# Kernel optimization log

Measured on AMD Instinct MI355X. Metric: run time of the kernel, lower is better.

Reference implementation:

```python
import jax, jax.numpy as jnp
import numpy as np

R = 100        # voxel grid resolution per axis
N = 200000     # number of active (non-empty) voxels
K = 3          # kernel size
CIN = 64
COUT = 64
NOFF = K ** 3 - 1  # 26 non-center offsets


def _build_maps():
    # Mirrors mapping_cuda: per kernel offset, find (input_row, output_row) pairs
    # such that coords[input] == coords[output] + offset (submanifold conv,
    # output coords == input coords).
    rng = np.random.default_rng(0)
    lin = rng.choice(R ** 3, size=N, replace=False)
    coords = np.stack(np.unravel_index(lin, (R, R, R)), axis=1)  # [N,3]
    lut = np.full(R ** 3, -1, dtype=np.int64)
    lut[lin] = np.arange(N)
    offs = [(dx, dy, dz) for dx in (-1, 0, 1) for dy in (-1, 0, 1)
            for dz in (-1, 0, 1) if (dx, dy, dz) != (0, 0, 0)]
    ins, outs = [], []
    for d in offs:
        tgt = coords - np.asarray(d)              # output coord receiving input i
        valid = np.all((tgt >= 0) & (tgt < R), axis=1)
        idx_i = np.nonzero(valid)[0]
        tlin = np.ravel_multi_index(tgt[valid].T, (R, R, R))
        j = lut[tlin]
        hit = j >= 0
        ins.append(idx_i[hit].astype(np.int32))
        outs.append(j[hit].astype(np.int32))
    P = max(len(a) for a in ins)
    imap = np.full((NOFF, P), -1, dtype=np.int32)
    omap = np.full((NOFF, P), -1, dtype=np.int32)
    for k, (a, b) in enumerate(zip(ins, outs)):
        imap[k, :len(a)] = a
        omap[k, :len(b)] = b
    return jnp.asarray(imap), jnp.asarray(omap)


def setup_inputs() -> dict:
    key = jax.random.key(0)
    kf, kw = jax.random.split(key)
    feats = jax.random.normal(kf, (N, CIN), dtype=jnp.float32)
    # reset_parameters: uniform(-stdv, stdv), stdv = 1/sqrt(out_channels * K^3)
    stdv = 1.0 / float(np.sqrt(COUT * K ** 3))
    kernel = jax.random.uniform(kw, (K ** 3, CIN, COUT), dtype=jnp.float32,
                                minval=-stdv, maxval=stdv)
    imap, omap = _build_maps()
    return {"feats": feats, "kernel": kernel, "imap": imap, "omap": omap}


def reference(feats, kernel, imap, omap):
    # Submanifold sparse 3D conv: gather -> per-offset GEMM -> scatter-add.
    K3 = kernel.shape[0]
    c = K3 // 2  # center offset: identity neighbor map
    w_nc = jnp.concatenate([kernel[:c], kernel[c + 1:]], axis=0)  # [26,Cin,Cout]
    mask = imap >= 0                                   # [26,P]
    gath = feats[jnp.where(mask, imap, 0)] * mask[..., None]   # [26,P,Cin]
    y = jnp.einsum('kpc,kco->kpo', gath, w_nc)         # [26,P,Cout]
    out = feats @ kernel[c]                            # center contribution [N,Cout]
    oi = jnp.where(mask, omap, 0).reshape(-1)          # masked rows add zeros at row 0
    out = out.at[oi].add(y.reshape(-1, y.shape[-1]))
    return out
```

## Files before the change

### kernel.cpp

```cpp
#include <hip/hip_runtime.h>


#define CIN 64
#define COUT 64
#define TR 32
#define NOFF 26

typedef short bf16x8 __attribute__((ext_vector_type(8)));
typedef unsigned short ushort8 __attribute__((ext_vector_type(8)));
typedef float f32x4 __attribute__((ext_vector_type(4)));

__device__ inline unsigned short bfbits(float f) {
    unsigned u = __builtin_bit_cast(unsigned, f);
    u += 0x7fffu + ((u >> 16) & 1u);
    return (unsigned short)(u >> 16);
}

__device__ inline int kk_of_item(int i) {
    return (i >= 26) ? 13 : 26 - (i < 13 ? i : i + 1);
}

__global__ __launch_bounds__(256) void prep_feats(const float* __restrict__ f,
                                                  unsigned short* __restrict__ fb,
                                                  int n) {
    const int i8 = (blockIdx.x * 256 + threadIdx.x) * 8;
    if (i8 >= n) return;
    const float4 v0 = *(const float4*)(f + i8);
    const float4 v1 = *(const float4*)(f + i8 + 4);
    union { unsigned short u[8]; bf16x8 v; } r;
    r.u[0] = bfbits(v0.x); r.u[1] = bfbits(v0.y);
    r.u[2] = bfbits(v0.z); r.u[3] = bfbits(v0.w);
    r.u[4] = bfbits(v1.x); r.u[5] = bfbits(v1.y);
    r.u[6] = bfbits(v1.z); r.u[7] = bfbits(v1.w);
    *(bf16x8*)(fb + i8) = r.v;
}

__global__ __launch_bounds__(256) void prep_wt(const float* __restrict__ W,
                                               unsigned short* __restrict__ Wt) {
    const int k = blockIdx.x;
    for (int idx = threadIdx.x; idx < CIN * COUT; idx += 256) {
        const int c = idx >> 6, o = idx & 63;
        const int q = c >> 3, e = c & 7;
        Wt[((k * 64 + o) * 64) + (((q ^ (o & 7)) << 3) + e)] =
            bfbits(W[(k * 64 + c) * 64 + o]);
    }
}

__global__ __launch_bounds__(256) void prep_tab_init(int* __restrict__ tab,
                                                     int nt, int N) {
    const size_t i4 = ((size_t)blockIdx.x * 256 + threadIdx.x) * 4;
    const size_t total = (size_t)27 * nt * TR;
    if (i4 >= total) return;
    const size_t mstep = (size_t)nt * TR;
    int4 v;
    int* vp = (int*)&v;
#pragma unroll
    for (int e = 0; e < 4; ++e) {
        const size_t l = i4 + e;
        const int m = (int)(l / mstep);
        const int r = (int)(l - (size_t)m * mstep);
        vp[e] = (m == 26 && r < N) ? r : N;
    }
    *(int4*)(tab + i4) = v;
}

__global__ __launch_bounds__(256) void prep_tab(const int* __restrict__ imap,
                                                const int* __restrict__ omap,
                                                int P, int nt,
                                                int* __restrict__ tab) {
    const int p = blockIdx.x * 256 + threadIdx.x;
    const int m = blockIdx.y;
    if (p >= P) return;
    const int iv = imap[(size_t)m * P + p];
    if (iv < 0) return;
    tab[((size_t)m * nt + (iv >> 5)) * TR + (iv & 31)] = omap[(size_t)m * P + p];
}

__global__ __launch_bounds__(256, 4) void spconv_v7(
    const unsigned short* __restrict__ fb,
    const unsigned short* __restrict__ wt,
    const int* __restrict__ tab,
    float* __restrict__ out, int N, int nt, int nwg)
{
    __shared__ unsigned short wbuf[2][4096];

    const int tid = threadIdx.x, w = tid >> 6, lane = tid & 63;
    const int col = lane & 15, grp = lane >> 4;

    const int orig = blockIdx.x;
    const int q = nwg >> 3, r8 = nwg & 7;
    const int xcd = orig & 7, k = orig >> 3;
    const int sb = (xcd < r8 ? xcd * (q + 1) : r8 * (q + 1) + (xcd - r8) * q) + k;

    const int t = sb * 4 + w;
    const int tt = (t < nt) ? t : (nt - 1);
    const int r0 = t * TR;
    const size_t tstep = (size_t)nt * TR;
    const int* tb = tab + (size_t)tt * TR + col;

#define TAB(j, s) tb[(size_t)((j) < 27 ? (j) : 26) * tstep + (s) * 16]

    int sv1[2], sv2[2], tvA[2], tvB[2];
    bf16x8 a0[2][2], a1[2][2], a2[2][2];
#pragma unroll
    for (int s = 0; s < 2; ++s) {
        const int sv0 = TAB(0, s);
        sv1[s] = TAB(1, s);
        sv2[s] = TAB(2, s);
        tvA[s] = TAB(3, s);
        tvB[s] = TAB(4, s);
        const bf16x8* fp = (const bf16x8*)(fb + (size_t)sv0 * 64 + grp * 8);
        a0[s][0] = fp[0];
        a0[s][1] = fp[4];
        const bf16x8* fq = (const bf16x8*)(fb + (size_t)sv1[s] * 64 + grp * 8);
        a1[s][0] = fq[0];
        a1[s][1] = fq[4];
    }

    {
        const unsigned short* wk = wt + kk_of_item(0) * 4096;
        const ushort8 wl0 = *(const ushort8*)(wk + tid * 8);
        const ushort8 wl1 = *(const ushort8*)(wk + 2048 + tid * 8);
        *(ushort8*)(&wbuf[0][tid * 8]) = wl0;
        *(ushort8*)(&wbuf[0][2048 + tid * 8]) = wl1;
    }
    asm volatile("s_waitcnt lgkmcnt(0)" ::: "memory");
    __builtin_amdgcn_s_barrier();

    f32x4 acc[2][4];
#pragma unroll
    for (int s = 0; s < 2; ++s)
#pragma unroll
        for (int ot = 0; ot < 4; ++ot) acc[s][ot] = {0.f, 0.f, 0.f, 0.f};

    for (int it = 0; it < 27; ++it) {
        const unsigned short* wkn = wt + kk_of_item(it + 1) * 4096;
        const ushort8 wl0 = *(const ushort8*)(wkn + tid * 8);
        const ushort8 wl1 = *(const ushort8*)(wkn + 2048 + tid * 8);

#pragma unroll
        for (int s = 0; s < 2; ++s) {
            const bf16x8* fp = (const bf16x8*)(fb + (size_t)sv2[s] * 64 + grp * 8);
            a2[s][0] = fp[0];
            a2[s][1] = fp[4];
        }

        int svn[2];
#pragma unroll
        for (int s = 0; s < 2; ++s) {
            svn[s] = tvA[s];
            tvA[s] = tvB[s];
            tvB[s] = TAB(it + 5, s);
        }

        const unsigned short* cb = wbuf[it & 1];
        __builtin_amdgcn_s_setprio(1);
#pragma unroll
        for (int ot = 0; ot < 4; ++ot) {
            const int o = ot * 16 + col;
            const bf16x8 b0 = *(const bf16x8*)(cb + o * 64 + ((grp ^ (col & 7)) << 3));
            const bf16x8 b1 = *(const bf16x8*)(cb + o * 64 + (((4 + grp) ^ (col & 7)) << 3));
#pragma unroll
            for (int s = 0; s < 2; ++s) {
                acc[s][ot] = __builtin_amdgcn_mfma_f32_16x16x32_bf16(a0[s][0], b0, acc[s][ot], 0, 0, 0);
                acc[s][ot] = __builtin_amdgcn_mfma_f32_16x16x32_bf16(a0[s][1], b1, acc[s][ot], 0, 0, 0);
            }
        }
        __builtin_amdgcn_s_setprio(0);

        unsigned short* nb = wbuf[(it + 1) & 1];
        *(ushort8*)(&nb[tid * 8]) = wl0;
        *(ushort8*)(&nb[2048 + tid * 8]) = wl1;

        asm volatile("s_waitcnt lgkmcnt(0)" ::: "memory");
        __builtin_amdgcn_s_barrier();

#pragma unroll
        for (int s = 0; s < 2; ++s) {
            a0[s][0] = a1[s][0]; a0[s][1] = a1[s][1];
            a1[s][0] = a2[s][0]; a1[s][1] = a2[s][1];
            sv2[s] = svn[s];
        }
    }

#pragma unroll
    for (int s = 0; s < 2; ++s)
#pragma unroll
        for (int ot = 0; ot < 4; ++ot) {
            const f32x4 cv = acc[s][ot];
#pragma unroll
            for (int reg = 0; reg < 4; ++reg) {
                const int rr = r0 + s * 16 + grp * 4 + reg;
                if (rr < N) out[(size_t)rr * 64 + ot * 16 + col] = cv[reg];
            }
        }
#undef TAB
}

template <int MODE>
__global__ __launch_bounds__(256) void spconv_fb(
    const float* __restrict__ feats, const float* __restrict__ W,
    const int* __restrict__ imap, const int* __restrict__ omap,
    float* __restrict__ out, int npairs)
{
    __shared__ float4 wt4[16 * 64];
    const int tid = threadIdx.x, koff = blockIdx.y;
    const float* Wk;
    const int* im = nullptr; const int* om = nullptr;
    if (MODE == 0) Wk = W + 13 * (CIN * COUT);
    else {
        const int kk = (koff < 13) ? koff : koff + 1;
        Wk = W + (size_t)kk * (CIN * COUT);
        im = imap + (size_t)koff * npairs; om = omap + (size_t)koff * npairs;
    }
    float* wts = (float*)wt4;
    for (int idx = tid; idx < CIN * COUT; idx += 256) {
        const int c = idx >> 6, o = idx & 63;
        wts[((c >> 2) * 64 + o) * 4 + (c & 3)] = Wk[idx];
    }
    __syncthreads();
    const int o = tid & 63, w = tid >> 6;
    const int base = blockIdx.x * 256 + w * 64;
    const float4* f4p = (const float4*)feats;
    for (int n = 0; n < 64; ++n) {
        const int p = base + n;
        if (p >= npairs) break;
        int i, j;
        if (MODE == 0) { i = p; j = p; }
        else { i = im[p]; if (i < 0) continue; j = om[p]; }
        i = __builtin_amdgcn_readfirstlane(i);
        float a = 0.f;
#pragma unroll
        for (int c4 = 0; c4 < 16; ++c4) {
            const float4 f = f4p[(size_t)i * 16 + c4];
            const float4 wv = wt4[c4 * 64 + o];
            a += f.x * wv.x + f.y * wv.y + f.z * wv.z + f.w * wv.w;
        }
        if (MODE == 0) out[(size_t)j * COUT + o] = a;
        else atomicAdd(&out[(size_t)j * COUT + o], a);
    }
}

extern "C" void kernel_launch(void* const* d_in, const int* in_sizes, int n_in,
                              void* d_out, int out_size, void* d_ws, size_t ws_size,
                              hipStream_t stream) {
    const float* feats = (const float*)d_in[0];
    const float* W     = (const float*)d_in[1];
    const int* imap    = (const int*)d_in[2];
    const int* omap    = (const int*)d_in[3];
    float* out         = (float*)d_out;

    const int N = in_sizes[0] / CIN;
    const int P = in_sizes[2] / NOFF;
    const int nt = (N + TR - 1) / TR;

    const size_t fb_bytes  = (size_t)(N + 1) * 64 * sizeof(unsigned short);
    const size_t wt_bytes  = 27 * 64 * 64 * sizeof(unsigned short);
    const size_t tab_bytes = (size_t)27 * nt * TR * sizeof(int);

    if (ws_size < fb_bytes + wt_bytes + tab_bytes) {
        dim3 blk(256);
        dim3 gc((N + 255) / 256, 1);
        spconv_fb<0><<<gc, blk, 0, stream>>>(feats, W, nullptr, nullptr, out, N);
        dim3 go((P + 255) / 256, NOFF);
        spconv_fb<1><<<go, blk, 0, stream>>>(feats, W, imap, omap, out, P);
        return;
    }

    unsigned short* fbp = (unsigned short*)d_ws;
    unsigned short* Wt  = (unsigned short*)((char*)d_ws + fb_bytes);
    int* tab            = (int*)((char*)d_ws + fb_bytes + wt_bytes);

    const int nf = N * 64;
    prep_feats<<<(nf / 8 + 255) / 256, 256, 0, stream>>>(feats, fbp, nf);
    hipMemsetAsync(fbp + (size_t)N * 64, 0, 128, stream);
    prep_wt<<<27, 256, 0, stream>>>(W, Wt);
    const size_t tot4 = (size_t)27 * nt * TR / 4;
    prep_tab_init<<<(int)((tot4 + 255) / 256), 256, 0, stream>>>(tab, nt, N);
    prep_tab<<<dim3((P + 255) / 256, NOFF), 256, 0, stream>>>(imap, omap, P, nt, tab);

    const int nwg = (nt + 3) / 4;
    spconv_v7<<<nwg, 256, 0, stream>>>(fbp, Wt, tab, out, N, nt, nwg);
}
```

Baseline: 107.7 us.

## Fully unroll offset loop with deeper weight prefetch and early LDS stores

The 27-step offset loop is fully unrolled. Gathered feature rows, table indices and weight tiles now live in per-step register arrays indexed at compile time, which removes the rotating-register copies. Global weight loads are issued two steps ahead instead of one. Each step writes the next weight tile into LDS before its MFMAs rather than after them, and the barrier after the last step is skipped. The aim is more latency hiding for the gather and weight loads, at the cost of a much larger code body and possible register pressure or spills under the 4-blocks-per-CU launch bound.

```diff
diff --git a/kernel.cpp b/kernel.cpp
--- a/kernel.cpp
+++ b/kernel.cpp
@@ -16,7 +16,7 @@
     return (unsigned short)(u >> 16);
 }
 
-__device__ inline int kk_of_item(int i) {
+__device__ inline constexpr int kk_of_item(int i) {
     return (i >= 26) ? 13 : 26 - (i < 13 ? i : i + 1);
 }
 
@@ -76,7 +76,7 @@
     tab[((size_t)m * nt + (iv >> 5)) * TR + (iv & 31)] = omap[(size_t)m * P + p];
 }
 
-__global__ __launch_bounds__(256, 4) void spconv_v7(
+__global__ __launch_bounds__(256, 4) void spconv_v8(
     const unsigned short* __restrict__ fb,
     const unsigned short* __restrict__ wt,
     const int* __restrict__ tab,
@@ -89,8 +89,8 @@
 
     const int orig = blockIdx.x;
     const int q = nwg >> 3, r8 = nwg & 7;
-    const int xcd = orig & 7, k = orig >> 3;
-    const int sb = (xcd < r8 ? xcd * (q + 1) : r8 * (q + 1) + (xcd - r8) * q) + k;
+    const int xcd = orig & 7, kb = orig >> 3;
+    const int sb = (xcd < r8 ? xcd * (q + 1) : r8 * (q + 1) + (xcd - r8) * q) + kb;
 
     const int t = sb * 4 + w;
     const int tt = (t < nt) ? t : (nt - 1);
@@ -98,31 +98,33 @@
     const size_t tstep = (size_t)nt * TR;
     const int* tb = tab + (size_t)tt * TR + col;
 
-#define TAB(j, s) tb[(size_t)((j) < 27 ? (j) : 26) * tstep + (s) * 16]
-
-    int sv1[2], sv2[2], tvA[2], tvB[2];
-    bf16x8 a0[2][2], a1[2][2], a2[2][2];
-#pragma unroll
-    for (int s = 0; s < 2; ++s) {
-        const int sv0 = TAB(0, s);
-        sv1[s] = TAB(1, s);
-        sv2[s] = TAB(2, s);
-        tvA[s] = TAB(3, s);
-        tvB[s] = TAB(4, s);
-        const bf16x8* fp = (const bf16x8*)(fb + (size_t)sv0 * 64 + grp * 8);
-        a0[s][0] = fp[0];
-        a0[s][1] = fp[4];
-        const bf16x8* fq = (const bf16x8*)(fb + (size_t)sv1[s] * 64 + grp * 8);
-        a1[s][0] = fq[0];
-        a1[s][1] = fq[4];
-    }
+    int svr[27][2];
+    bf16x8 af[27][2][2];
+    ushort8 wr[27][2];
+
+#pragma unroll
+    for (int j = 0; j < 4; ++j)
+#pragma unroll
+        for (int s = 0; s < 2; ++s) svr[j][s] = tb[(size_t)j * tstep + s * 16];
+
+#pragma unroll
+    for (int j = 0; j < 2; ++j)
+#pragma unroll
+        for (int s = 0; s < 2; ++s) {
+            const bf16x8* fp = (const bf16x8*)(fb + (size_t)svr[j][s] * 64 + grp * 8);
+            af[j][s][0] = fp[0];
+            af[j][s][1] = fp[4];
+        }
 
     {
-        const unsigned short* wk = wt + kk_of_item(0) * 4096;
-        const ushort8 wl0 = *(const ushort8*)(wk + tid * 8);
-        const ushort8 wl1 = *(const ushort8*)(wk + 2048 + tid * 8);
-        *(ushort8*)(&wbuf[0][tid * 8]) = wl0;
-        *(ushort8*)(&wbuf[0][2048 + tid * 8]) = wl1;
+        const unsigned short* wk0 = wt + kk_of_item(0) * 4096;
+        const ushort8 t0 = *(const ushort8*)(wk0 + tid * 8);
+        const ushort8 t1 = *(const ushort8*)(wk0 + 2048 + tid * 8);
+        const unsigned short* wk1 = wt + kk_of_item(1) * 4096;
+        wr[1][0] = *(const ushort8*)(wk1 + tid * 8);
+        wr[1][1] = *(const ushort8*)(wk1 + 2048 + tid * 8);
+        *(ushort8*)(&wbuf[0][tid * 8]) = t0;
+        *(ushort8*)(&wbuf[0][2048 + tid * 8]) = t1;
     }
     asm volatile("s_waitcnt lgkmcnt(0)" ::: "memory");
     __builtin_amdgcn_s_barrier();
@@ -133,26 +135,31 @@
 #pragma unroll
         for (int ot = 0; ot < 4; ++ot) acc[s][ot] = {0.f, 0.f, 0.f, 0.f};
 
+#pragma unroll
     for (int it = 0; it < 27; ++it) {
-        const unsigned short* wkn = wt + kk_of_item(it + 1) * 4096;
-        const ushort8 wl0 = *(const ushort8*)(wkn + tid * 8);
-        const ushort8 wl1 = *(const ushort8*)(wkn + 2048 + tid * 8);
-
-#pragma unroll
-        for (int s = 0; s < 2; ++s) {
-            const bf16x8* fp = (const bf16x8*)(fb + (size_t)sv2[s] * 64 + grp * 8);
-            a2[s][0] = fp[0];
-            a2[s][1] = fp[4];
-        }
-
-        int svn[2];
-#pragma unroll
-        for (int s = 0; s < 2; ++s) {
-            svn[s] = tvA[s];
-            tvA[s] = tvB[s];
-            tvB[s] = TAB(it + 5, s);
-        }
-
+        if (it + 2 <= 26) {
+            const unsigned short* wk = wt + kk_of_item(it + 2) * 4096;
+            wr[it + 2][0] = *(const ushort8*)(wk + tid * 8);
+            wr[it + 2][1] = *(const ushort8*)(wk + 2048 + tid * 8);
+        }
+        if (it + 2 <= 26) {
+#pragma unroll
+            for (int s = 0; s < 2; ++s) {
+                const bf16x8* fp = (const bf16x8*)(fb + (size_t)svr[it + 2][s] * 64 + grp * 8);
+                af[it + 2][s][0] = fp[0];
+                af[it + 2][s][1] = fp[4];
+            }
+        }
+        if (it + 4 <= 26) {
+#pragma unroll
+            for (int s = 0; s < 2; ++s)
+                svr[it + 4][s] = tb[(size_t)(it + 4) * tstep + s * 16];
+        }
+        if (it + 1 <= 26) {
+            unsigned short* nb = wbuf[(it + 1) & 1];
+            *(ushort8*)(&nb[tid * 8]) = wr[it + 1][0];
+            *(ushort8*)(&nb[2048 + tid * 8]) = wr[it + 1][1];
+        }
         const unsigned short* cb = wbuf[it & 1];
         __builtin_amdgcn_s_setprio(1);
 #pragma unroll
@@ -162,24 +169,14 @@
             const bf16x8 b1 = *(const bf16x8*)(cb + o * 64 + (((4 + grp) ^ (col & 7)) << 3));
 #pragma unroll
             for (int s = 0; s < 2; ++s) {
-                acc[s][ot] = __builtin_amdgcn_mfma_f32_16x16x32_bf16(a0[s][0], b0, acc[s][ot], 0, 0, 0);
-                acc[s][ot] = __builtin_amdgcn_mfma_f32_16x16x32_bf16(a0[s][1], b1, acc[s][ot], 0, 0, 0);
+                acc[s][ot] = __builtin_amdgcn_mfma_f32_16x16x32_bf16(af[it][s][0], b0, acc[s][ot], 0, 0, 0);
+                acc[s][ot] = __builtin_amdgcn_mfma_f32_16x16x32_bf16(af[it][s][1], b1, acc[s][ot], 0, 0, 0);
             }
         }
         __builtin_amdgcn_s_setprio(0);
-
-        unsigned short* nb = wbuf[(it + 1) & 1];
-        *(ushort8*)(&nb[tid * 8]) = wl0;
-        *(ushort8*)(&nb[2048 + tid * 8]) = wl1;
-
-        asm volatile("s_waitcnt lgkmcnt(0)" ::: "memory");
-        __builtin_amdgcn_s_barrier();
-
-#pragma unroll
-        for (int s = 0; s < 2; ++s) {
-            a0[s][0] = a1[s][0]; a0[s][1] = a1[s][1];
-            a1[s][0] = a2[s][0]; a1[s][1] = a2[s][1];
-            sv2[s] = svn[s];
+        if (it < 26) {
+            asm volatile("s_waitcnt lgkmcnt(0)" ::: "memory");
+            __builtin_amdgcn_s_barrier();
         }
     }
 
@@ -194,7 +191,6 @@
                 if (rr < N) out[(size_t)rr * 64 + ot * 16 + col] = cv[reg];
             }
         }
-#undef TAB
 }
 
 template <int MODE>
@@ -280,5 +276,5 @@
     prep_tab<<<dim3((P + 255) / 256, NOFF), 256, 0, stream>>>(imap, omap, P, nt, tab);
 
     const int nwg = (nt + 3) / 4;
-    spconv_v7<<<nwg, 256, 0, stream>>>(fbp, Wt, tab, out, N, nt, nwg);
-}
+    spconv_v8<<<nwg, 256, 0, stream>>>(fbp, Wt, tab, out, N, nt, nwg);
+}
```

Result: faster. 98.13 us (-8.9%).
